# Optimization experiments

Hardware: AMD Instinct MI355X
Metric: run time of the kernel (lower is better)

Reference implementation:

```python
import jax, jax.numpy as jnp
import numpy as np

B, S, DIM, H = 2, 2048, 512, 8  # batch, seq_len, model dim, num_heads


def setup_inputs() -> dict:
    key = jax.random.key(0)
    ks = jax.random.split(key, 8)
    s = 0.02
    return {
        "queries": jax.random.normal(ks[0], (B, S, DIM), dtype=jnp.float32),
        "keys": jax.random.normal(ks[1], (B, S, DIM), dtype=jnp.float32),
        "Wq": jax.random.normal(ks[2], (DIM, DIM), dtype=jnp.float32) * s,
        "bq": jax.random.normal(ks[3], (DIM,), dtype=jnp.float32) * s,
        "Wk": jax.random.normal(ks[4], (DIM, DIM), dtype=jnp.float32) * s,
        "bk": jax.random.normal(ks[5], (DIM,), dtype=jnp.float32) * s,
        "Wv": jax.random.normal(ks[6], (DIM, DIM), dtype=jnp.float32) * s,
        "bv": jax.random.normal(ks[7], (DIM,), dtype=jnp.float32) * s,
        "causality": 1,
    }


def _split_heads(x):
    # torch: cat(chunk(x, H, dim=2), dim=0): [B,S,D] -> [H*B, S, d], head-major
    b, s, dmod = x.shape
    d = dmod // H
    return x.reshape(b, s, H, d).transpose(2, 0, 1, 3).reshape(H * b, s, d)


def reference(queries, keys, Wq, bq, Wk, bk, Wv, bv, causality):
    b, sq, dim = queries.shape
    sk = keys.shape[1]
    d = dim // H

    Q = queries @ Wq.T + bq
    K = keys @ Wk.T + bk
    V = keys @ Wv.T + bv
    Q_, K_, V_ = _split_heads(Q), _split_heads(K), _split_heads(V)  # [H*B, S, d]

    scores = jnp.einsum("nqd,nkd->nqk", Q_, K_) / jnp.sqrt(jnp.float32(d))

    # key padding mask from raw keys: sign(sum |keys|) -> [B,Sk] -> [H*B,1,Sk]
    key_masks = jnp.sign(jnp.sum(jnp.abs(keys), axis=-1))
    key_masks = jnp.tile(key_masks, (H, 1))[:, None, :]
    scores = jnp.where(key_masks == 0, -jnp.inf, scores)

    if causality:
        tril = jnp.tril(jnp.ones((sq, sk), dtype=bool))
        scores = jnp.where(tril[None, :, :], scores, -jnp.inf)

    attn = jax.nn.softmax(scores, axis=-1)
    attn = jnp.nan_to_num(attn, nan=0.0, posinf=0.0, neginf=0.0)

    # query padding mask: [B,Sq] -> [H*B,Sq,1], multiplicative
    query_masks = jnp.sign(jnp.sum(jnp.abs(queries), axis=-1))
    query_masks = jnp.tile(query_masks, (H, 1))[:, :, None]
    attn = attn * query_masks

    # attention_weights: stack H chunks along dim 1 -> [B, H, Sq, Sk]
    attention_weights = attn.reshape(H, b, sq, sk).transpose(1, 0, 2, 3)

    # dropout in eval mode = identity
    out = jnp.einsum("nqk,nkd->nqd", attn, V_)  # [H*B, Sq, d]
    # merge heads back: cat(chunk(out, H, dim=0), dim=2)
    out = out.reshape(H, b, sq, d).transpose(1, 2, 0, 3).reshape(b, sq, dim)
    return out, attention_weights
```

## Files before the change

### kernel.cpp

```cpp
#include <hip/hip_runtime.h>
#include <math.h>

#define B_ 2
#define S_ 2048
#define DIM_ 512
#define H_ 8
#define DH_ 64

typedef __bf16 bf16x8 __attribute__((ext_vector_type(8)));
typedef float f32x4 __attribute__((ext_vector_type(4)));
typedef float vf4 __attribute__((ext_vector_type(4)));
typedef unsigned short ushort_t;
typedef ushort_t ushort8 __attribute__((ext_vector_type(8)));

__device__ __forceinline__ ushort_t f2bf(float f) {
    union { float f; unsigned u; } v; v.f = f;
    unsigned u = v.u;
    return (ushort_t)((u + 0x7FFFu + ((u >> 16) & 1u)) >> 16);
}

__global__ __launch_bounds__(256) void convert_kernel(
    const float* __restrict__ q, const float* __restrict__ k,
    const float* __restrict__ wq, const float* __restrict__ wk,
    const float* __restrict__ wv,
    ushort_t* qbf, ushort_t* kbf, ushort_t* wqb, ushort_t* wkb, ushort_t* wvb)
{
    const float* src; ushort_t* dst; int n;
    switch (blockIdx.y) {
        case 0: src = q;  dst = qbf; n = B_ * S_ * DIM_; break;
        case 1: src = k;  dst = kbf; n = B_ * S_ * DIM_; break;
        case 2: src = wq; dst = wqb; n = DIM_ * DIM_; break;
        case 3: src = wk; dst = wkb; n = DIM_ * DIM_; break;
        default: src = wv; dst = wvb; n = DIM_ * DIM_; break;
    }
    int i4 = blockIdx.x * 256 + threadIdx.x;
    if (i4 * 4 >= n) return;
    float4 v = ((const float4*)src)[i4];
    ushort4 o;
    o.x = f2bf(v.x); o.y = f2bf(v.y); o.z = f2bf(v.z); o.w = f2bf(v.w);
    ((ushort4*)dst)[i4] = o;
}

__global__ __launch_bounds__(256) void proj_mfma_kernel(
    const ushort_t* __restrict__ Qin, const ushort_t* __restrict__ Kin,
    const ushort_t* __restrict__ Wqb, const float* __restrict__ bq,
    const ushort_t* __restrict__ Wkb, const float* __restrict__ bk,
    const ushort_t* __restrict__ Wvb, const float* __restrict__ bv,
    ushort_t* __restrict__ Qh, ushort_t* __restrict__ Kh, ushort_t* __restrict__ Vt)
{
    __shared__ float T[128][68];

    const int which = blockIdx.z;
    const ushort_t* A = (which == 0) ? Qin : Kin;
    const ushort_t* W = (which == 0) ? Wqb : (which == 1 ? Wkb : Wvb);
    const float* bias = (which == 0) ? bq : (which == 1 ? bk : bv);

    const int r0 = blockIdx.x * 128;
    const int h  = blockIdx.y;
    const int c0 = h * DH_;
    const int tid = threadIdx.x;
    const int w = tid >> 6, l = tid & 63;
    const int lr = l & 15, lg = l >> 4;

    f32x4 acc[2][4] = {};
    const ushort_t* arow0 = A + (size_t)(r0 + w * 32 + lr) * DIM_ + lg * 8;
    const ushort_t* arow1 = arow0 + (size_t)16 * DIM_;
    const ushort_t* wrow0 = W + (size_t)(c0 + lr) * DIM_ + lg * 8;

#pragma unroll 4
    for (int ks = 0; ks < DIM_ / 32; ++ks) {
        bf16x8 a0 = *(const bf16x8*)(arow0 + ks * 32);
        bf16x8 a1 = *(const bf16x8*)(arow1 + ks * 32);
#pragma unroll
        for (int ct = 0; ct < 4; ++ct) {
            bf16x8 bfr = *(const bf16x8*)(wrow0 + (size_t)ct * 16 * DIM_ + ks * 32);
            acc[0][ct] = __builtin_amdgcn_mfma_f32_16x16x32_bf16(a0, bfr, acc[0][ct], 0, 0, 0);
            acc[1][ct] = __builtin_amdgcn_mfma_f32_16x16x32_bf16(a1, bfr, acc[1][ct], 0, 0, 0);
        }
    }

    const int bb = r0 >> 11;
    const int s0 = r0 & (S_ - 1);
    const int n = h * B_ + bb;

    if (which < 2) {
        ushort_t* OUT = (which == 0) ? Qh : Kh;
#pragma unroll
        for (int rg = 0; rg < 2; ++rg) {
#pragma unroll
            for (int ct = 0; ct < 4; ++ct) {
                int d = ct * 16 + lr;
                float bi = bias[c0 + d];
#pragma unroll
                for (int reg = 0; reg < 4; ++reg) {
                    int s = s0 + w * 32 + rg * 16 + lg * 4 + reg;
                    OUT[((size_t)n * S_ + s) * DH_ + d] = f2bf(acc[rg][ct][reg] + bi);
                }
            }
        }
    } else {
#pragma unroll
        for (int rg = 0; rg < 2; ++rg) {
#pragma unroll
            for (int ct = 0; ct < 4; ++ct) {
                int d = ct * 16 + lr;
                float bi = bias[c0 + d];
#pragma unroll
                for (int reg = 0; reg < 4; ++reg)
                    T[w * 32 + rg * 16 + lg * 4 + reg][d] = acc[rg][ct][reg] + bi;
            }
        }
        __syncthreads();
        int d = tid & 63, sc = tid >> 6;
        ushort8 o[4];
#pragma unroll
        for (int i = 0; i < 32; ++i)
            ((ushort_t*)o)[i] = f2bf(T[sc * 32 + i][d]);
        ushort8* dst = (ushort8*)(Vt + ((size_t)n * DH_ + d) * S_ + s0 + sc * 32);
        dst[0] = o[0]; dst[1] = o[1]; dst[2] = o[2]; dst[3] = o[3];
    }
}

__global__ __launch_bounds__(64) void attn_mfma_kernel(
    const ushort_t* __restrict__ Qh, const ushort_t* __restrict__ Kh,
    const ushort_t* __restrict__ Vt, const int* __restrict__ causp,
    float* __restrict__ outp, float* __restrict__ attnw)
{
    __shared__ ushort_t Pscr[16][40];

    const int bid = blockIdx.x;
    const int x = bid & 7, i = bid >> 3;
    const int n  = x * 2 + (i & 1);
    const int qt = 127 - (i >> 1);
    const int h = n / B_, b = n % B_;
    const int q0 = qt * 16;
    const int l = threadIdx.x;
    const int lr = l & 15, lg = l >> 4;
    const int causal = causp[0];

    const int kend = causal ? (((q0 + 47) >> 5) << 5) : S_;
    const int q_g = q0 + lr;

    float* attrow = attnw + ((size_t)((b * H_ + h) * S_ + q0)) * S_;

    if (causal && kend < S_) {
        vf4 z = {0.f, 0.f, 0.f, 0.f};
        for (int r = 0; r < 16; ++r) {
            float* ar = attrow + (size_t)r * S_;
            for (int c = kend + l * 4; c < S_; c += 256)
                __builtin_nontemporal_store(z, (vf4*)&ar[c]);
        }
    }

    const ushort_t* qrow = Qh + ((size_t)n * S_ + q0 + lr) * DH_ + lg * 8;
    bf16x8 qa0 = *(const bf16x8*)(qrow);
    bf16x8 qa1 = *(const bf16x8*)(qrow + 32);
    const ushort_t* Kbase = Kh + (size_t)n * S_ * DH_;
    const ushort_t* Vbase = Vt + (size_t)n * DH_ * S_;

    float pl = 0.f;
    {
        const ushort_t* kr = Kbase + (size_t)lr * DH_ + lg * 8;
        bf16x8 ka0 = *(const bf16x8*)(kr);
        bf16x8 ka1 = *(const bf16x8*)(kr + 32);
        bf16x8 kb0 = *(const bf16x8*)(kr + 16 * DH_);
        bf16x8 kb1 = *(const bf16x8*)(kr + 16 * DH_ + 32);
        for (int kc = 0; kc < kend; kc += 32) {
            const int kn = (kc + 32 < kend) ? kc + 32 : kc;
            const ushort_t* krn = Kbase + (size_t)(kn + lr) * DH_ + lg * 8;
            bf16x8 na0 = *(const bf16x8*)(krn);
            bf16x8 na1 = *(const bf16x8*)(krn + 32);
            bf16x8 nb0 = *(const bf16x8*)(krn + 16 * DH_);
            bf16x8 nb1 = *(const bf16x8*)(krn + 16 * DH_ + 32);
            f32x4 a0 = {}, a1 = {};
            a0 = __builtin_amdgcn_mfma_f32_16x16x32_bf16(ka0, qa0, a0, 0, 0, 0);
            a0 = __builtin_amdgcn_mfma_f32_16x16x32_bf16(ka1, qa1, a0, 0, 0, 0);
            a1 = __builtin_amdgcn_mfma_f32_16x16x32_bf16(kb0, qa0, a1, 0, 0, 0);
            a1 = __builtin_amdgcn_mfma_f32_16x16x32_bf16(kb1, qa1, a1, 0, 0, 0);
            if (causal && kc + 32 >= kend) {
#pragma unroll
                for (int reg = 0; reg < 4; ++reg) {
                    int k0 = kc + lg * 4 + reg;
                    float e0 = (k0 <= q_g)      ? __expf(a0[reg] * 0.125f) : 0.f;
                    float e1 = (k0 + 16 <= q_g) ? __expf(a1[reg] * 0.125f) : 0.f;
                    pl += e0 + e1;
                }
            } else {
#pragma unroll
                for (int reg = 0; reg < 4; ++reg)
                    pl += __expf(a0[reg] * 0.125f) + __expf(a1[reg] * 0.125f);
            }
            ka0 = na0; ka1 = na1; kb0 = nb0; kb1 = nb1;
        }
    }
    pl += __shfl_xor(pl, 16);
    pl += __shfl_xor(pl, 32);
    const float inv = 1.f / pl;

    f32x4 oacc[4] = {};
    {
        const ushort_t* kr = Kbase + (size_t)lr * DH_ + lg * 8;
        bf16x8 ka0 = *(const bf16x8*)(kr);
        bf16x8 ka1 = *(const bf16x8*)(kr + 32);
        bf16x8 kb0 = *(const bf16x8*)(kr + 16 * DH_);
        bf16x8 kb1 = *(const bf16x8*)(kr + 16 * DH_ + 32);
        for (int kc = 0; kc < kend; kc += 32) {
            const int kn = (kc + 32 < kend) ? kc + 32 : kc;
            const ushort_t* krn = Kbase + (size_t)(kn + lr) * DH_ + lg * 8;
            bf16x8 na0 = *(const bf16x8*)(krn);
            bf16x8 na1 = *(const bf16x8*)(krn + 32);
            bf16x8 nb0 = *(const bf16x8*)(krn + 16 * DH_);
            bf16x8 nb1 = *(const bf16x8*)(krn + 16 * DH_ + 32);
            f32x4 a0 = {}, a1 = {};
            a0 = __builtin_amdgcn_mfma_f32_16x16x32_bf16(ka0, qa0, a0, 0, 0, 0);
            a0 = __builtin_amdgcn_mfma_f32_16x16x32_bf16(ka1, qa1, a0, 0, 0, 0);
            a1 = __builtin_amdgcn_mfma_f32_16x16x32_bf16(kb0, qa0, a1, 0, 0, 0);
            a1 = __builtin_amdgcn_mfma_f32_16x16x32_bf16(kb1, qa1, a1, 0, 0, 0);

            vf4 p0, p1; ushort4 u0, u1;
            const bool msk = causal && (kc + 32 >= kend);
#pragma unroll
            for (int reg = 0; reg < 4; ++reg) {
                float e0 = __expf(a0[reg] * 0.125f) * inv;
                float e1 = __expf(a1[reg] * 0.125f) * inv;
                if (msk) {
                    if (kc + lg * 4 + reg > q_g)      e0 = 0.f;
                    if (kc + 16 + lg * 4 + reg > q_g) e1 = 0.f;
                }
                p0[reg] = e0; p1[reg] = e1;
                __bf16 t0 = (__bf16)e0, t1 = (__bf16)e1;
                ((ushort_t*)&u0)[reg] = *(ushort_t*)&t0;
                ((ushort_t*)&u1)[reg] = *(ushort_t*)&t1;
            }
            __builtin_nontemporal_store(p0, (vf4*)&attrow[(size_t)lr * S_ + kc + lg * 4]);
            __builtin_nontemporal_store(p1, (vf4*)&attrow[(size_t)lr * S_ + kc + 16 + lg * 4]);

            *(ushort4*)&Pscr[lr][lg * 4]      = u0;
            *(ushort4*)&Pscr[lr][16 + lg * 4] = u1;
            bf16x8 pa = *(const bf16x8*)&Pscr[lr][lg * 8];
#pragma unroll
            for (int dt = 0; dt < 4; ++dt) {
                bf16x8 vb = *(const bf16x8*)(Vbase + (size_t)(dt * 16 + lr) * S_ + kc + lg * 8);
                oacc[dt] = __builtin_amdgcn_mfma_f32_16x16x32_bf16(pa, vb, oacc[dt], 0, 0, 0);
            }
            ka0 = na0; ka1 = na1; kb0 = nb0; kb1 = nb1;
        }
    }

#pragma unroll
    for (int dt = 0; dt < 4; ++dt)
#pragma unroll
        for (int reg = 0; reg < 4; ++reg) {
            int qq = q0 + lg * 4 + reg;
            __builtin_nontemporal_store(oacc[dt][reg],
                &outp[((size_t)b * S_ + qq) * DIM_ + h * DH_ + dt * 16 + lr]);
        }
}

extern "C" void kernel_launch(void* const* d_in, const int* in_sizes, int n_in,
                              void* d_out, int out_size, void* d_ws, size_t ws_size,
                              hipStream_t stream) {
    const float* queries = (const float*)d_in[0];
    const float* keys    = (const float*)d_in[1];
    const float* Wq = (const float*)d_in[2];
    const float* bq = (const float*)d_in[3];
    const float* Wk = (const float*)d_in[4];
    const float* bk = (const float*)d_in[5];
    const float* Wv = (const float*)d_in[6];
    const float* bv = (const float*)d_in[7];
    const int*   caus = (const int*)d_in[8];

    char* ws = (char*)d_ws;
    ushort_t* Qin_bf = (ushort_t*)ws;  ws += (size_t)B_*S_*DIM_*2;
    ushort_t* Kin_bf = (ushort_t*)ws;  ws += (size_t)B_*S_*DIM_*2;
    ushort_t* Wqb = (ushort_t*)ws;     ws += (size_t)DIM_*DIM_*2;
    ushort_t* Wkb = (ushort_t*)ws;     ws += (size_t)DIM_*DIM_*2;
    ushort_t* Wvb = (ushort_t*)ws;     ws += (size_t)DIM_*DIM_*2;
    ushort_t* Qh = (ushort_t*)ws;      ws += (size_t)H_*B_*S_*DH_*2;
    ushort_t* Kh = (ushort_t*)ws;      ws += (size_t)H_*B_*S_*DH_*2;
    ushort_t* Vt = (ushort_t*)ws;      ws += (size_t)H_*B_*DH_*S_*2;

    float* outp  = (float*)d_out;
    float* attnw = outp + (size_t)B_ * S_ * DIM_;

    convert_kernel<<<dim3(2048, 5), 256, 0, stream>>>(
        queries, keys, Wq, Wk, Wv, Qin_bf, Kin_bf, Wqb, Wkb, Wvb);

    proj_mfma_kernel<<<dim3(32, 8, 3), 256, 0, stream>>>(
        Qin_bf, Kin_bf, Wqb, bq, Wkb, bk, Wvb, bv, Qh, Kh, Vt);

    attn_mfma_kernel<<<2048, 64, 0, stream>>>(Qh, Kh, Vt, caus, outp, attnw);
}
```

Before: 178.5 us.

## Single-pass attention with bf16 scratch probabilities and a separate normalize-stream kernel

```diff
diff --git a/kernel.cpp b/kernel.cpp
--- a/kernel.cpp
+++ b/kernel.cpp
@@ -17,6 +17,10 @@
     union { float f; unsigned u; } v; v.f = f;
     unsigned u = v.u;
     return (ushort_t)((u + 0x7FFFu + ((u >> 16) & 1u)) >> 16);
+}
+__device__ __forceinline__ float bf2f(ushort_t u) {
+    union { unsigned u; float f; } v; v.u = ((unsigned)u) << 16;
+    return v.f;
 }
 
 __global__ __launch_bounds__(256) void convert_kernel(
@@ -121,10 +125,11 @@
     }
 }
 
-__global__ __launch_bounds__(64) void attn_mfma_kernel(
+__global__ __launch_bounds__(64) void attn_core_kernel(
     const ushort_t* __restrict__ Qh, const ushort_t* __restrict__ Kh,
     const ushort_t* __restrict__ Vt, const int* __restrict__ causp,
-    float* __restrict__ outp, float* __restrict__ attnw)
+    float* __restrict__ outp, float* __restrict__ attnw,
+    float* __restrict__ inv_ws)
 {
     __shared__ ushort_t Pscr[16][40];
 
@@ -142,15 +147,7 @@
     const int q_g = q0 + lr;
 
     float* attrow = attnw + ((size_t)((b * H_ + h) * S_ + q0)) * S_;
-
-    if (causal && kend < S_) {
-        vf4 z = {0.f, 0.f, 0.f, 0.f};
-        for (int r = 0; r < 16; ++r) {
-            float* ar = attrow + (size_t)r * S_;
-            for (int c = kend + l * 4; c < S_; c += 256)
-                __builtin_nontemporal_store(z, (vf4*)&ar[c]);
-        }
-    }
+    ushort_t* prow = (ushort_t*)(attrow + (size_t)lr * S_);
 
     const ushort_t* qrow = Qh + ((size_t)n * S_ + q0 + lr) * DH_ + lg * 8;
     bf16x8 qa0 = *(const bf16x8*)(qrow);
@@ -159,12 +156,18 @@
     const ushort_t* Vbase = Vt + (size_t)n * DH_ * S_;
 
     float pl = 0.f;
+    f32x4 oacc[4] = {};
     {
         const ushort_t* kr = Kbase + (size_t)lr * DH_ + lg * 8;
         bf16x8 ka0 = *(const bf16x8*)(kr);
         bf16x8 ka1 = *(const bf16x8*)(kr + 32);
         bf16x8 kb0 = *(const bf16x8*)(kr + 16 * DH_);
         bf16x8 kb1 = *(const bf16x8*)(kr + 16 * DH_ + 32);
+        bf16x8 va[4];
+#pragma unroll
+        for (int dt = 0; dt < 4; ++dt)
+            va[dt] = *(const bf16x8*)(Vbase + (size_t)(dt * 16 + lr) * S_ + lg * 8);
+
         for (int kc = 0; kc < kend; kc += 32) {
             const int kn = (kc + 32 < kend) ? kc + 32 : kc;
             const ushort_t* krn = Kbase + (size_t)(kn + lr) * DH_ + lg * 8;
@@ -172,89 +175,98 @@
             bf16x8 na1 = *(const bf16x8*)(krn + 32);
             bf16x8 nb0 = *(const bf16x8*)(krn + 16 * DH_);
             bf16x8 nb1 = *(const bf16x8*)(krn + 16 * DH_ + 32);
+            bf16x8 nva[4];
+#pragma unroll
+            for (int dt = 0; dt < 4; ++dt)
+                nva[dt] = *(const bf16x8*)(Vbase + (size_t)(dt * 16 + lr) * S_ + kn + lg * 8);
+
             f32x4 a0 = {}, a1 = {};
             a0 = __builtin_amdgcn_mfma_f32_16x16x32_bf16(ka0, qa0, a0, 0, 0, 0);
             a0 = __builtin_amdgcn_mfma_f32_16x16x32_bf16(ka1, qa1, a0, 0, 0, 0);
             a1 = __builtin_amdgcn_mfma_f32_16x16x32_bf16(kb0, qa0, a1, 0, 0, 0);
             a1 = __builtin_amdgcn_mfma_f32_16x16x32_bf16(kb1, qa1, a1, 0, 0, 0);
-            if (causal && kc + 32 >= kend) {
-#pragma unroll
-                for (int reg = 0; reg < 4; ++reg) {
-                    int k0 = kc + lg * 4 + reg;
-                    float e0 = (k0 <= q_g)      ? __expf(a0[reg] * 0.125f) : 0.f;
-                    float e1 = (k0 + 16 <= q_g) ? __expf(a1[reg] * 0.125f) : 0.f;
-                    pl += e0 + e1;
-                }
-            } else {
-#pragma unroll
-                for (int reg = 0; reg < 4; ++reg)
-                    pl += __expf(a0[reg] * 0.125f) + __expf(a1[reg] * 0.125f);
-            }
-            ka0 = na0; ka1 = na1; kb0 = nb0; kb1 = nb1;
-        }
-    }
-    pl += __shfl_xor(pl, 16);
-    pl += __shfl_xor(pl, 32);
-    const float inv = 1.f / pl;
-
-    f32x4 oacc[4] = {};
-    {
-        const ushort_t* kr = Kbase + (size_t)lr * DH_ + lg * 8;
-        bf16x8 ka0 = *(const bf16x8*)(kr);
-        bf16x8 ka1 = *(const bf16x8*)(kr + 32);
-        bf16x8 kb0 = *(const bf16x8*)(kr + 16 * DH_);
-        bf16x8 kb1 = *(const bf16x8*)(kr + 16 * DH_ + 32);
-        for (int kc = 0; kc < kend; kc += 32) {
-            const int kn = (kc + 32 < kend) ? kc + 32 : kc;
-            const ushort_t* krn = Kbase + (size_t)(kn + lr) * DH_ + lg * 8;
-            bf16x8 na0 = *(const bf16x8*)(krn);
-            bf16x8 na1 = *(const bf16x8*)(krn + 32);
-            bf16x8 nb0 = *(const bf16x8*)(krn + 16 * DH_);
-            bf16x8 nb1 = *(const bf16x8*)(krn + 16 * DH_ + 32);
-            f32x4 a0 = {}, a1 = {};
-            a0 = __builtin_amdgcn_mfma_f32_16x16x32_bf16(ka0, qa0, a0, 0, 0, 0);
-            a0 = __builtin_amdgcn_mfma_f32_16x16x32_bf16(ka1, qa1, a0, 0, 0, 0);
-            a1 = __builtin_amdgcn_mfma_f32_16x16x32_bf16(kb0, qa0, a1, 0, 0, 0);
-            a1 = __builtin_amdgcn_mfma_f32_16x16x32_bf16(kb1, qa1, a1, 0, 0, 0);
-
-            vf4 p0, p1; ushort4 u0, u1;
+
+            ushort4 u0, u1;
             const bool msk = causal && (kc + 32 >= kend);
 #pragma unroll
             for (int reg = 0; reg < 4; ++reg) {
-                float e0 = __expf(a0[reg] * 0.125f) * inv;
-                float e1 = __expf(a1[reg] * 0.125f) * inv;
+                float e0 = __expf(a0[reg] * 0.125f);
+                float e1 = __expf(a1[reg] * 0.125f);
                 if (msk) {
                     if (kc + lg * 4 + reg > q_g)      e0 = 0.f;
                     if (kc + 16 + lg * 4 + reg > q_g) e1 = 0.f;
                 }
-                p0[reg] = e0; p1[reg] = e1;
+                pl += e0 + e1;
                 __bf16 t0 = (__bf16)e0, t1 = (__bf16)e1;
                 ((ushort_t*)&u0)[reg] = *(ushort_t*)&t0;
                 ((ushort_t*)&u1)[reg] = *(ushort_t*)&t1;
             }
-            __builtin_nontemporal_store(p0, (vf4*)&attrow[(size_t)lr * S_ + kc + lg * 4]);
-            __builtin_nontemporal_store(p1, (vf4*)&attrow[(size_t)lr * S_ + kc + 16 + lg * 4]);
+            *(ushort4*)&prow[kc + lg * 4]      = u0;
+            *(ushort4*)&prow[kc + 16 + lg * 4] = u1;
 
             *(ushort4*)&Pscr[lr][lg * 4]      = u0;
             *(ushort4*)&Pscr[lr][16 + lg * 4] = u1;
             bf16x8 pa = *(const bf16x8*)&Pscr[lr][lg * 8];
 #pragma unroll
-            for (int dt = 0; dt < 4; ++dt) {
-                bf16x8 vb = *(const bf16x8*)(Vbase + (size_t)(dt * 16 + lr) * S_ + kc + lg * 8);
-                oacc[dt] = __builtin_amdgcn_mfma_f32_16x16x32_bf16(pa, vb, oacc[dt], 0, 0, 0);
-            }
+            for (int dt = 0; dt < 4; ++dt)
+                oacc[dt] = __builtin_amdgcn_mfma_f32_16x16x32_bf16(pa, va[dt], oacc[dt], 0, 0, 0);
+
             ka0 = na0; ka1 = na1; kb0 = nb0; kb1 = nb1;
-        }
-    }
-
+#pragma unroll
+            for (int dt = 0; dt < 4; ++dt) va[dt] = nva[dt];
+        }
+    }
+
+    pl += __shfl_xor(pl, 16);
+    pl += __shfl_xor(pl, 32);
+    const float inv = 1.f / pl;
+    if (lg == 0) inv_ws[n * S_ + q0 + lr] = inv;
+
+    float inv_r[4];
+#pragma unroll
+    for (int reg = 0; reg < 4; ++reg)
+        inv_r[reg] = __shfl(inv, lg * 4 + reg, 64);
 #pragma unroll
     for (int dt = 0; dt < 4; ++dt)
 #pragma unroll
         for (int reg = 0; reg < 4; ++reg) {
             int qq = q0 + lg * 4 + reg;
-            __builtin_nontemporal_store(oacc[dt][reg],
-                &outp[((size_t)b * S_ + qq) * DIM_ + h * DH_ + dt * 16 + lr]);
-        }
+            outp[((size_t)b * S_ + qq) * DIM_ + h * DH_ + dt * 16 + lr] =
+                oacc[dt][reg] * inv_r[reg];
+        }
+}
+
+__global__ __launch_bounds__(256) void attn_stream_kernel(
+    const float* __restrict__ inv_ws, const int* __restrict__ causp,
+    float* __restrict__ attnw)
+{
+    const int bid = blockIdx.x;
+    const int x = bid & 7;
+    const int ridx = bid >> 3;
+    const int n = x * 2 + (ridx & 1);
+    const int q = ridx >> 1;
+    const int h = n / B_, b = n % B_;
+    const int causal = causp[0];
+    const int kend = causal ? (((((q >> 4) << 4) + 47) >> 5) << 5) : S_;
+    const int t = threadIdx.x;
+    const int c = t * 8;
+
+    float* ar = attnw + ((size_t)(b * H_ + h) * S_ + q) * S_;
+    const float inv = inv_ws[n * S_ + q];
+
+    ushort8 v = {};
+    if (c < kend) v = *(const ushort8*)((const ushort_t*)ar + c);
+    __syncthreads();
+
+    vf4 o0 = {0.f, 0.f, 0.f, 0.f}, o1 = {0.f, 0.f, 0.f, 0.f};
+    if (c < kend) {
+        o0.x = bf2f(v[0]) * inv; o0.y = bf2f(v[1]) * inv;
+        o0.z = bf2f(v[2]) * inv; o0.w = bf2f(v[3]) * inv;
+        o1.x = bf2f(v[4]) * inv; o1.y = bf2f(v[5]) * inv;
+        o1.z = bf2f(v[6]) * inv; o1.w = bf2f(v[7]) * inv;
+    }
+    *(vf4*)&ar[c] = o0;
+    *(vf4*)&ar[c + 4] = o1;
 }
 
 extern "C" void kernel_launch(void* const* d_in, const int* in_sizes, int n_in,
@@ -279,6 +291,7 @@
     ushort_t* Qh = (ushort_t*)ws;      ws += (size_t)H_*B_*S_*DH_*2;
     ushort_t* Kh = (ushort_t*)ws;      ws += (size_t)H_*B_*S_*DH_*2;
     ushort_t* Vt = (ushort_t*)ws;      ws += (size_t)H_*B_*DH_*S_*2;
+    float* inv_ws = (float*)ws;        ws += (size_t)H_*B_*S_*4;
 
     float* outp  = (float*)d_out;
     float* attnw = outp + (size_t)B_ * S_ * DIM_;
@@ -289,5 +302,7 @@
     proj_mfma_kernel<<<dim3(32, 8, 3), 256, 0, stream>>>(
         Qin_bf, Kin_bf, Wqb, bq, Wkb, bk, Wvb, bv, Qh, Kh, Vt);
 
-    attn_mfma_kernel<<<2048, 64, 0, stream>>>(Qh, Kh, Vt, caus, outp, attnw);
-}
+    attn_core_kernel<<<2048, 64, 0, stream>>>(Qh, Kh, Vt, caus, outp, attnw, inv_ws);
+
+    attn_stream_kernel<<<H_ * B_ * S_, 256, 0, stream>>>(inv_ws, caus, attnw);
+}
```

After: 177.9 us. Within noise of the previous version (-0.4%).
